# Kernel optimization log

Hardware: AMD Instinct MI355X
Metric: run time of the kernel (lower is better)

## Reference

```python
import jax, jax.numpy as jnp
import numpy as np

N = 50000      # number of nodes
D = 128        # embedding dim
K = 16         # padded neighbors per node
B = 100000     # number of train pairs
LAYERS = 2     # convolution layers


def setup_inputs() -> dict:
    key = jax.random.key(0)
    k_pairs, k_lab, k_nbr, k_emb, k_w1, k_w2 = jax.random.split(key, 6)
    pairs = jax.random.randint(k_pairs, (B, 2), 0, N, dtype=jnp.int64 if jax.config.jax_enable_x64 else jnp.int32)
    labels = jax.random.randint(k_lab, (B,), 0, 2, dtype=jnp.int32)
    neighbors = jax.random.randint(k_nbr, (N, K), 0, N, dtype=jnp.int32)
    embedding = jax.random.normal(k_emb, (N, D), dtype=jnp.float32)
    W1 = jax.random.normal(k_w1, (2 * D, D), dtype=jnp.float32) * (1.0 / np.sqrt(2 * D))
    b1 = jnp.zeros((D,), dtype=jnp.float32)
    W2 = jax.random.normal(k_w2, (D, 2), dtype=jnp.float32) * (1.0 / np.sqrt(D))
    b2 = jnp.zeros((2,), dtype=jnp.float32)
    return {"pairs": pairs, "labels": labels, "neighbors": neighbors,
            "embedding": embedding, "W1": W1, "b1": b1, "W2": W2, "b2": b2}


def _aggregate(embedding, neighbors):
    # Multi-layer mean neighbor aggregation over all N nodes.
    H = embedding
    for _ in range(LAYERS):
        # gather [N, K, D] then mean over neighbors -> [N, D]
        H = jnp.take(H, neighbors, axis=0).mean(axis=1)
    return H


def reference(pairs, labels, neighbors, embedding, W1, b1, W2, b2):
    H = _aggregate(embedding, neighbors)           # [N, D]
    src = jnp.take(H, pairs[:, 0], axis=0)         # [B, D]
    dst = jnp.take(H, pairs[:, 1], axis=0)         # [B, D]
    x = jnp.concatenate([src, dst], axis=-1)       # [B, 2D]
    h = jax.nn.relu(x @ W1 + b1)                   # [B, D]
    logits = h @ W2 + b2                           # [B, 2]
    # Original applies Softmax, then CrossEntropyLoss (which log_softmaxes again).
    probs = jax.nn.softmax(logits, axis=-1)
    logp = jax.nn.log_softmax(probs, axis=-1)
    loss = -jnp.take_along_axis(logp, labels[:, None].astype(jnp.int32), axis=1).mean()
    return loss
```

## Files before the change

### kernel.cpp

```cpp
#include <hip/hip_runtime.h>
#include <hip/hip_bf16.h>

#define NNODES 50000
#define DIM    128
#define KNBR   16
#define NPAIRS 100000
#define MBLK   128

typedef float          f32x4  __attribute__((ext_vector_type(4)));
typedef float          f32x2  __attribute__((ext_vector_type(2)));
typedef __bf16         bf16x8 __attribute__((ext_vector_type(8)));
typedef unsigned short u16x8  __attribute__((ext_vector_type(8)));
typedef unsigned int   u32x2  __attribute__((ext_vector_type(2)));

__device__ __forceinline__ unsigned short f2bf(float f) {
    unsigned int u = __builtin_bit_cast(unsigned int, f);
    u = (u + 0x7fffu + ((u >> 16) & 1u)) >> 16;
    return (unsigned short)u;
}

#if __has_builtin(__builtin_amdgcn_cvt_pk_f32_fp8) && __has_builtin(__builtin_amdgcn_cvt_pk_fp8_f32)
template <bool HI>
__device__ __forceinline__ f32x2 fp8x2_dec(unsigned int w) {
    return __builtin_amdgcn_cvt_pk_f32_fp8((int)w, HI);
}
template <bool HI>
__device__ __forceinline__ unsigned int fp8x2_enc(float a, float b, unsigned int old) {
    return (unsigned int)__builtin_amdgcn_cvt_pk_fp8_f32(a, b, (int)old, HI);
}
#else
__device__ __forceinline__ float e4m3_dec1(unsigned int b) {
    unsigned int s = (b & 0x80u) << 24;
    unsigned int em = b & 0x7fu;
    float mag = (em >= 8u)
        ? __builtin_bit_cast(float, (((em >> 3) + 120u) << 23) | ((em & 7u) << 20))
        : (float)em * 0.001953125f;
    return __builtin_bit_cast(float, __builtin_bit_cast(unsigned int, mag) | s);
}
template <bool HI>
__device__ __forceinline__ f32x2 fp8x2_dec(unsigned int w) {
    unsigned int v = HI ? (w >> 16) : w;
    f32x2 r; r[0] = e4m3_dec1(v & 0xffu); r[1] = e4m3_dec1((v >> 8) & 0xffu);
    return r;
}
__device__ __forceinline__ unsigned int e4m3_enc1(float f) {
    unsigned int s = (__builtin_bit_cast(unsigned int, f) >> 24) & 0x80u;
    float af = fminf(fabsf(f), 448.0f);
    unsigned int u = __builtin_bit_cast(unsigned int, af);
    int e = (int)(u >> 23) - 127;
    if (e < -9) return s;
    if (e < -6) {
        int q = (int)rintf(af * 512.0f);
        return s | (unsigned int)q;
    }
    unsigned int mant = u & 0x7fffffu;
    unsigned int r = (mant + 0x7ffffu + ((mant >> 20) & 1u)) >> 20;
    unsigned int out = (((unsigned int)(e + 7)) << 3) + r;
    if (out > 0x7eu) out = 0x7eu;
    return s | out;
}
template <bool HI>
__device__ __forceinline__ unsigned int fp8x2_enc(float a, float b, unsigned int old) {
    unsigned int p = e4m3_enc1(a) | (e4m3_enc1(b) << 8);
    return HI ? ((old & 0x0000ffffu) | (p << 16)) : ((old & 0xffff0000u) | p);
}
#endif

#define AS1 __attribute__((address_space(1)))
#define AS3 __attribute__((address_space(3)))
__device__ __forceinline__ void gload_lds16(const void* g, void* l) {
    __builtin_amdgcn_global_load_lds((AS1 void*)(g), (AS3 void*)(l), 16, 0, 0);
}

__global__ void w1t_kernel(const float* __restrict__ W1, unsigned short* __restrict__ W1t) {
    int g = blockIdx.x * 256 + threadIdx.x;
    int i = g >> 7;
    int d = g & 127;
    W1t[d * 256 + i] = f2bf(W1[g]);
}

__global__ void e2f8_kernel(const float* __restrict__ E, unsigned int* __restrict__ E8) {
    int g = blockIdx.x * 256 + threadIdx.x;
    const f32x4 v0 = *(const f32x4*)(E + (size_t)g * 8);
    const f32x4 v1 = *(const f32x4*)(E + (size_t)g * 8 + 4);
    unsigned int w0 = 0, w1 = 0;
    w0 = fp8x2_enc<false>(v0[0], v0[1], w0);
    w0 = fp8x2_enc<true >(v0[2], v0[3], w0);
    w1 = fp8x2_enc<false>(v1[0], v1[1], w1);
    w1 = fp8x2_enc<true >(v1[2], v1[3], w1);
    u32x2 o; o[0] = w0; o[1] = w1;
    *(u32x2*)(E8 + (size_t)g * 2) = o;
}

__global__ void agg1_kernel(const unsigned char* __restrict__ E8, const int* __restrict__ nbr,
                            unsigned char* __restrict__ H1f8) {
    int t = threadIdx.x;
    int node = blockIdx.x * 16 + (t >> 4);
    int c = t & 15;
    const int* nl = nbr + node * KNBR;
    float a[8] = {0.f,0.f,0.f,0.f,0.f,0.f,0.f,0.f};
#pragma unroll
    for (int k = 0; k < KNBR; ++k) {
        const u32x2 w = *(const u32x2*)(E8 + (size_t)nl[k] * 128 + c * 8);
        f32x2 f;
        f = fp8x2_dec<false>(w[0]); a[0] += f[0]; a[1] += f[1];
        f = fp8x2_dec<true >(w[0]); a[2] += f[0]; a[3] += f[1];
        f = fp8x2_dec<false>(w[1]); a[4] += f[0]; a[5] += f[1];
        f = fp8x2_dec<true >(w[1]); a[6] += f[0]; a[7] += f[1];
    }
    unsigned int w0 = 0, w1 = 0;
    w0 = fp8x2_enc<false>(a[0] * 0.0625f, a[1] * 0.0625f, w0);
    w0 = fp8x2_enc<true >(a[2] * 0.0625f, a[3] * 0.0625f, w0);
    w1 = fp8x2_enc<false>(a[4] * 0.0625f, a[5] * 0.0625f, w1);
    w1 = fp8x2_enc<true >(a[6] * 0.0625f, a[7] * 0.0625f, w1);
    u32x2 o; o[0] = w0; o[1] = w1;
    *(u32x2*)(H1f8 + (size_t)node * 128 + c * 8) = o;
}

__global__ void agg2_kernel(const unsigned char* __restrict__ H1f8, const int* __restrict__ nbr,
                            unsigned short* __restrict__ H2b) {
    int t = threadIdx.x;
    int node = blockIdx.x * 16 + (t >> 4);
    int c = t & 15;
    const int* nl = nbr + node * KNBR;
    float a[8] = {0.f,0.f,0.f,0.f,0.f,0.f,0.f,0.f};
#pragma unroll
    for (int k = 0; k < KNBR; ++k) {
        const u32x2 w = *(const u32x2*)(H1f8 + (size_t)nl[k] * 128 + c * 8);
        f32x2 f;
        f = fp8x2_dec<false>(w[0]); a[0] += f[0]; a[1] += f[1];
        f = fp8x2_dec<true >(w[0]); a[2] += f[0]; a[3] += f[1];
        f = fp8x2_dec<false>(w[1]); a[4] += f[0]; a[5] += f[1];
        f = fp8x2_dec<true >(w[1]); a[6] += f[0]; a[7] += f[1];
    }
    u16x8 o;
#pragma unroll
    for (int j = 0; j < 8; ++j) o[j] = f2bf(a[j] * 0.0625f);
    *(u16x8*)(H2b + (size_t)node * DIM + c * 8) = o;
}

__global__ __launch_bounds__(256, 2) void pair_mlp_kernel(
    const int* __restrict__ pairs, const int* __restrict__ labels,
    const unsigned short* __restrict__ H2b, const unsigned short* __restrict__ W1t,
    const float* __restrict__ b1, const float* __restrict__ W2,
    const float* __restrict__ b2, float* __restrict__ out) {
    __shared__ unsigned short As[MBLK * 256];
    __shared__ float LP[4][MBLK][2];
    __shared__ float wred[4];

    const int t    = threadIdx.x;
    const int wave = t >> 6;
    const int lane = t & 63;
    const int base = blockIdx.x * MBLK;

    const int lq = (lane & 31) * 16;
    const int lr = lane >> 5;

#pragma unroll
    for (int i = 0; i < 16; ++i) {
        int m0 = wave * 32 + i * 2;
        int m  = m0 + lr;
        int b  = lq ^ ((m & 7) << 4);
        int half = lq >> 8;
        int pm = base + m; if (pm >= NPAIRS) pm = NPAIRS - 1;
        int node = pairs[pm * 2 + half];
        gload_lds16((const char*)H2b + (size_t)node * 256 + (b & 255),
                    (char*)As + m0 * 512);
    }

    const int lg = lane >> 4;
    const int ll = lane & 15;
    const int col0 = wave * 32 + ll;
    const int col1 = col0 + 16;
    bf16x8 breg0[8], breg1[8];
#pragma unroll
    for (int ks = 0; ks < 8; ++ks) {
        const int kb = ks * 64 + lg * 16;
        breg0[ks] = *(const bf16x8*)((const char*)W1t + col0 * 512 + kb);
        breg1[ks] = *(const bf16x8*)((const char*)W1t + col1 * 512 + kb);
    }
    __syncthreads();

    f32x4 acc[8][2];
    {
        f32x4 z = {0.f, 0.f, 0.f, 0.f};
#pragma unroll
        for (int i = 0; i < 8; ++i) { acc[i][0] = z; acc[i][1] = z; }
    }
#pragma unroll
    for (int ks = 0; ks < 8; ++ks) {
        const int kb = ks * 64 + lg * 16;
#pragma unroll
        for (int mf = 0; mf < 8; ++mf) {
            int row = mf * 16 + ll;
            bf16x8 af = *(const bf16x8*)((const char*)As + row * 512 + (kb ^ ((row & 7) << 4)));
            acc[mf][0] = __builtin_amdgcn_mfma_f32_16x16x32_bf16(af, breg0[ks], acc[mf][0], 0, 0, 0);
            acc[mf][1] = __builtin_amdgcn_mfma_f32_16x16x32_bf16(af, breg1[ks], acc[mf][1], 0, 0, 0);
        }
    }

    {
        const float b1v0 = b1[col0], b1v1 = b1[col1];
        const float w2a0 = W2[col0 * 2], w2b0 = W2[col0 * 2 + 1];
        const float w2a1 = W2[col1 * 2], w2b1 = W2[col1 * 2 + 1];
#pragma unroll
        for (int mf = 0; mf < 8; ++mf) {
            float p0[4], p1[4];
#pragma unroll
            for (int r = 0; r < 4; ++r) {
                float h0 = fmaxf(acc[mf][0][r] + b1v0, 0.f);
                float h1 = fmaxf(acc[mf][1][r] + b1v1, 0.f);
                p0[r] = h0 * w2a0 + h1 * w2a1;
                p1[r] = h0 * w2b0 + h1 * w2b1;
            }
#pragma unroll
            for (int s = 1; s < 16; s <<= 1) {
#pragma unroll
                for (int r = 0; r < 4; ++r) {
                    p0[r] += __shfl_xor(p0[r], s, 16);
                    p1[r] += __shfl_xor(p1[r], s, 16);
                }
            }
            if (ll == 0) {
                int rb = mf * 16 + lg * 4;
#pragma unroll
                for (int r = 0; r < 4; ++r) {
                    LP[wave][rb + r][0] = p0[r];
                    LP[wave][rb + r][1] = p1[r];
                }
            }
        }
    }
    __syncthreads();

    float myloss = 0.f;
    if (t < MBLK) {
        int pm = base + t;
        if (pm < NPAIRS) {
            float l0 = b2[0] + LP[0][t][0] + LP[1][t][0] + LP[2][t][0] + LP[3][t][0];
            float l1 = b2[1] + LP[0][t][1] + LP[1][t][1] + LP[2][t][1] + LP[3][t][1];
            float mx = fmaxf(l0, l1);
            float e0 = __expf(l0 - mx), e1 = __expf(l1 - mx);
            float inv = 1.f / (e0 + e1);
            float q0 = e0 * inv, q1 = e1 * inv;
            float lse2 = __logf(__expf(q0) + __expf(q1));
            myloss = lse2 - (labels[pm] ? q1 : q0);
        }
    }
#pragma unroll
    for (int s = 1; s < 64; s <<= 1) myloss += __shfl_xor(myloss, s, 64);
    if (lane == 0) wred[wave] = myloss;
    __syncthreads();
    if (t == 0)
        atomicAdd(out, (wred[0] + wred[1] + wred[2] + wred[3]) * (1.0f / (float)NPAIRS));
}

extern "C" void kernel_launch(void* const* d_in, const int* in_sizes, int n_in,
                              void* d_out, int out_size, void* d_ws, size_t ws_size,
                              hipStream_t stream) {
    const int*   pairs  = (const int*)d_in[0];
    const int*   labels = (const int*)d_in[1];
    const int*   nbr    = (const int*)d_in[2];
    const float* E      = (const float*)d_in[3];
    const float* W1     = (const float*)d_in[4];
    const float* b1     = (const float*)d_in[5];
    const float* W2     = (const float*)d_in[6];
    const float* b2     = (const float*)d_in[7];
    float* out = (float*)d_out;

    char* ws = (char*)d_ws;
    unsigned short* W1t  = (unsigned short*)(ws);
    unsigned char*  E8   = (unsigned char*)(ws + 65536);
    unsigned char*  H1f8 = E8 + (size_t)NNODES * DIM;
    unsigned short* H2b  = (unsigned short*)(H1f8 + (size_t)NNODES * DIM);

    (void)hipMemsetAsync(out, 0, sizeof(float), stream);

    w1t_kernel<<<dim3(128), dim3(256), 0, stream>>>(W1, W1t);
    e2f8_kernel<<<dim3((NNODES * DIM) / (256 * 8)), dim3(256), 0, stream>>>(E, (unsigned int*)E8);
    agg1_kernel<<<dim3(NNODES / 16), dim3(256), 0, stream>>>(E8, nbr, H1f8);
    agg2_kernel<<<dim3(NNODES / 16), dim3(256), 0, stream>>>(H1f8, nbr, H2b);
    pair_mlp_kernel<<<dim3((NPAIRS + MBLK - 1) / MBLK), dim3(256), 0, stream>>>(
        pairs, labels, H2b, W1t, b1, W2, b2, out);
}
```

Measured before the change: 144.6 us.

## Persist pair MLP blocks with double-buffered gathers; stage aggregation rows through LDS

The pair MLP kernel becomes persistent: 512 blocks each loop over 64-pair tiles. The next tile's H2 row gather goes into a second LDS buffer while MFMAs run on the current one, and W1 is loaded into registers once per block instead of once per tile. The aggregation kernels now issue all neighbor row loads as asynchronous global-to-LDS copies before any accumulation, so more loads are in flight per wave. The cost is extra LDS, more barriers per tile and added per-block control logic.

```diff
diff --git a/kernel.cpp b/kernel.cpp
--- a/kernel.cpp
+++ b/kernel.cpp
@@ -5,13 +5,16 @@
 #define DIM    128
 #define KNBR   16
 #define NPAIRS 100000
-#define MBLK   128
+#define MBLK   64
+#define NT     1563
+#define GRID_P 512
 
 typedef float          f32x4  __attribute__((ext_vector_type(4)));
 typedef float          f32x2  __attribute__((ext_vector_type(2)));
 typedef __bf16         bf16x8 __attribute__((ext_vector_type(8)));
 typedef unsigned short u16x8  __attribute__((ext_vector_type(8)));
 typedef unsigned int   u32x2  __attribute__((ext_vector_type(2)));
+typedef unsigned int   u32x4  __attribute__((ext_vector_type(4)));
 
 __device__ __forceinline__ unsigned short f2bf(float f) {
     unsigned int u = __builtin_bit_cast(unsigned int, f);
@@ -49,10 +52,7 @@
     unsigned int u = __builtin_bit_cast(unsigned int, af);
     int e = (int)(u >> 23) - 127;
     if (e < -9) return s;
-    if (e < -6) {
-        int q = (int)rintf(af * 512.0f);
-        return s | (unsigned int)q;
-    }
+    if (e < -6) { int q = (int)rintf(af * 512.0f); return s | (unsigned int)q; }
     unsigned int mant = u & 0x7fffffu;
     unsigned int r = (mant + 0x7ffffu + ((mant >> 20) & 1u)) >> 20;
     unsigned int out = (((unsigned int)(e + 7)) << 3) + r;
@@ -92,51 +92,67 @@
     *(u32x2*)(E8 + (size_t)g * 2) = o;
 }
 
-__global__ void agg1_kernel(const unsigned char* __restrict__ E8, const int* __restrict__ nbr,
-                            unsigned char* __restrict__ H1f8) {
-    int t = threadIdx.x;
-    int node = blockIdx.x * 16 + (t >> 4);
-    int c = t & 15;
-    const int* nl = nbr + node * KNBR;
-    float a[8] = {0.f,0.f,0.f,0.f,0.f,0.f,0.f,0.f};
+__device__ __forceinline__ void agg_core(const unsigned char* __restrict__ T,
+                                         const int* __restrict__ nbr,
+                                         unsigned char* lds_wave,
+                                         int node_base,
+                                         int lane, float* a ) {
+    const int rsub = lane >> 3;
+    const int bcol = (lane & 7) * 16;
+    const int* nb = nbr + node_base * KNBR;
+#pragma unroll
+    for (int i = 0; i < 8; ++i) {
+        int nl = nb[i * 8 + rsub];
+        gload_lds16(T + (size_t)nl * 128 + bcol, lds_wave + i * 1024);
+    }
+    asm volatile("s_waitcnt vmcnt(0)" ::: "memory");
+    __builtin_amdgcn_sched_barrier(0);
+    const int g = lane >> 4;
+    const int c = lane & 15;
+#pragma unroll
+    for (int j = 0; j < 8; ++j) a[j] = 0.f;
 #pragma unroll
     for (int k = 0; k < KNBR; ++k) {
-        const u32x2 w = *(const u32x2*)(E8 + (size_t)nl[k] * 128 + c * 8);
+        const u32x2 v = *(const u32x2*)(lds_wave + (g * 16 + k) * 128 + c * 8);
         f32x2 f;
-        f = fp8x2_dec<false>(w[0]); a[0] += f[0]; a[1] += f[1];
-        f = fp8x2_dec<true >(w[0]); a[2] += f[0]; a[3] += f[1];
-        f = fp8x2_dec<false>(w[1]); a[4] += f[0]; a[5] += f[1];
-        f = fp8x2_dec<true >(w[1]); a[6] += f[0]; a[7] += f[1];
-    }
-    unsigned int w0 = 0, w1 = 0;
-    w0 = fp8x2_enc<false>(a[0] * 0.0625f, a[1] * 0.0625f, w0);
-    w0 = fp8x2_enc<true >(a[2] * 0.0625f, a[3] * 0.0625f, w0);
-    w1 = fp8x2_enc<false>(a[4] * 0.0625f, a[5] * 0.0625f, w1);
-    w1 = fp8x2_enc<true >(a[6] * 0.0625f, a[7] * 0.0625f, w1);
-    u32x2 o; o[0] = w0; o[1] = w1;
-    *(u32x2*)(H1f8 + (size_t)node * 128 + c * 8) = o;
-}
-
-__global__ void agg2_kernel(const unsigned char* __restrict__ H1f8, const int* __restrict__ nbr,
-                            unsigned short* __restrict__ H2b) {
-    int t = threadIdx.x;
-    int node = blockIdx.x * 16 + (t >> 4);
-    int c = t & 15;
-    const int* nl = nbr + node * KNBR;
-    float a[8] = {0.f,0.f,0.f,0.f,0.f,0.f,0.f,0.f};
-#pragma unroll
-    for (int k = 0; k < KNBR; ++k) {
-        const u32x2 w = *(const u32x2*)(H1f8 + (size_t)nl[k] * 128 + c * 8);
-        f32x2 f;
-        f = fp8x2_dec<false>(w[0]); a[0] += f[0]; a[1] += f[1];
-        f = fp8x2_dec<true >(w[0]); a[2] += f[0]; a[3] += f[1];
-        f = fp8x2_dec<false>(w[1]); a[4] += f[0]; a[5] += f[1];
-        f = fp8x2_dec<true >(w[1]); a[6] += f[0]; a[7] += f[1];
-    }
+        f = fp8x2_dec<false>(v[0]); a[0] += f[0]; a[1] += f[1];
+        f = fp8x2_dec<true >(v[0]); a[2] += f[0]; a[3] += f[1];
+        f = fp8x2_dec<false>(v[1]); a[4] += f[0]; a[5] += f[1];
+        f = fp8x2_dec<true >(v[1]); a[6] += f[0]; a[7] += f[1];
+    }
+}
+
+__global__ __launch_bounds__(256) void agg1_kernel(const unsigned char* __restrict__ E8,
+                                                   const int* __restrict__ nbr,
+                                                   unsigned char* __restrict__ H1f8) {
+    __shared__ unsigned char SL[4][8192];
+    const int t = threadIdx.x, wave = t >> 6, lane = t & 63;
+    const int node_base = blockIdx.x * 16 + wave * 4;
+    float a[8];
+    agg_core(E8, nbr, SL[wave], node_base, lane, a);
+    const int g = lane >> 4, c = lane & 15;
+    unsigned int o0 = 0, o1 = 0;
+    o0 = fp8x2_enc<false>(a[0] * 0.0625f, a[1] * 0.0625f, o0);
+    o0 = fp8x2_enc<true >(a[2] * 0.0625f, a[3] * 0.0625f, o0);
+    o1 = fp8x2_enc<false>(a[4] * 0.0625f, a[5] * 0.0625f, o1);
+    o1 = fp8x2_enc<true >(a[6] * 0.0625f, a[7] * 0.0625f, o1);
+    u32x2 o; o[0] = o0; o[1] = o1;
+    *(u32x2*)(H1f8 + (size_t)(node_base + g) * 128 + c * 8) = o;
+}
+
+__global__ __launch_bounds__(256) void agg2_kernel(const unsigned char* __restrict__ H1f8,
+                                                   const int* __restrict__ nbr,
+                                                   unsigned short* __restrict__ H2b) {
+    __shared__ unsigned char SL[4][8192];
+    const int t = threadIdx.x, wave = t >> 6, lane = t & 63;
+    const int node_base = blockIdx.x * 16 + wave * 4;
+    float a[8];
+    agg_core(H1f8, nbr, SL[wave], node_base, lane, a);
+    const int g = lane >> 4, c = lane & 15;
     u16x8 o;
 #pragma unroll
     for (int j = 0; j < 8; ++j) o[j] = f2bf(a[j] * 0.0625f);
-    *(u16x8*)(H2b + (size_t)node * DIM + c * 8) = o;
+    *(u16x8*)(H2b + (size_t)(node_base + g) * DIM + c * 8) = o;
 }
 
 __global__ __launch_bounds__(256, 2) void pair_mlp_kernel(
@@ -144,34 +160,37 @@
     const unsigned short* __restrict__ H2b, const unsigned short* __restrict__ W1t,
     const float* __restrict__ b1, const float* __restrict__ W2,
     const float* __restrict__ b2, float* __restrict__ out) {
-    __shared__ unsigned short As[MBLK * 256];
+    __shared__ unsigned short As[2][MBLK * 256];
     __shared__ float LP[4][MBLK][2];
     __shared__ float wred[4];
 
-    const int t    = threadIdx.x;
-    const int wave = t >> 6;
-    const int lane = t & 63;
-    const int base = blockIdx.x * MBLK;
-
-    const int lq = (lane & 31) * 16;
-    const int lr = lane >> 5;
-
-#pragma unroll
-    for (int i = 0; i < 16; ++i) {
-        int m0 = wave * 32 + i * 2;
-        int m  = m0 + lr;
-        int b  = lq ^ ((m & 7) << 4);
-        int half = lq >> 8;
-        int pm = base + m; if (pm >= NPAIRS) pm = NPAIRS - 1;
-        int node = pairs[pm * 2 + half];
-        gload_lds16((const char*)H2b + (size_t)node * 256 + (b & 255),
-                    (char*)As + m0 * 512);
-    }
-
-    const int lg = lane >> 4;
-    const int ll = lane & 15;
+    const int tid  = threadIdx.x;
+    const int wave = tid >> 6;
+    const int lane = tid & 63;
+    const int bid  = blockIdx.x;
+
+    const int lq   = (lane & 31) * 16;
+    const int lr   = lane >> 5;
+    const int half = lq >> 8;
+    const int lg   = lane >> 4;
+    const int ll   = lane & 15;
     const int col0 = wave * 32 + ll;
     const int col1 = col0 + 16;
+    const int myN  = (NT - bid + GRID_P - 1) / GRID_P;
+
+    const float b1v0 = b1[col0], b1v1 = b1[col1];
+    const float w2a0 = W2[col0 * 2], w2b0 = W2[col0 * 2 + 1];
+    const float w2a1 = W2[col1 * 2], w2b1 = W2[col1 * 2 + 1];
+    const float b20 = b2[0], b21 = b2[1];
+    int lab[4] = {0, 0, 0, 0};
+#pragma unroll
+    for (int j = 0; j < 4; ++j) {
+        int tt = bid + j * GRID_P;
+        if (tt < NT && tid < MBLK) {
+            int pm = tt * MBLK + tid;
+            if (pm < NPAIRS) lab[j] = labels[pm];
+        }
+    }
     bf16x8 breg0[8], breg1[8];
 #pragma unroll
     for (int ks = 0; ks < 8; ++ks) {
@@ -179,32 +198,67 @@
         breg0[ks] = *(const bf16x8*)((const char*)W1t + col0 * 512 + kb);
         breg1[ks] = *(const bf16x8*)((const char*)W1t + col1 * 512 + kb);
     }
-    __syncthreads();
-
-    f32x4 acc[8][2];
-    {
-        f32x4 z = {0.f, 0.f, 0.f, 0.f};
-#pragma unroll
-        for (int i = 0; i < 8; ++i) { acc[i][0] = z; acc[i][1] = z; }
-    }
-#pragma unroll
-    for (int ks = 0; ks < 8; ++ks) {
-        const int kb = ks * 64 + lg * 16;
-#pragma unroll
-        for (int mf = 0; mf < 8; ++mf) {
-            int row = mf * 16 + ll;
-            bf16x8 af = *(const bf16x8*)((const char*)As + row * 512 + (kb ^ ((row & 7) << 4)));
-            acc[mf][0] = __builtin_amdgcn_mfma_f32_16x16x32_bf16(af, breg0[ks], acc[mf][0], 0, 0, 0);
-            acc[mf][1] = __builtin_amdgcn_mfma_f32_16x16x32_bf16(af, breg1[ks], acc[mf][1], 0, 0, 0);
-        }
-    }
-
-    {
-        const float b1v0 = b1[col0], b1v1 = b1[col1];
-        const float w2a0 = W2[col0 * 2], w2b0 = W2[col0 * 2 + 1];
-        const float w2a1 = W2[col1 * 2], w2b1 = W2[col1 * 2 + 1];
-#pragma unroll
-        for (int mf = 0; mf < 8; ++mf) {
+#pragma unroll
+    for (int i = 0; i < 8; ++i) {
+        int m0 = wave * 16 + i * 2;
+        int m  = m0 + lr;
+        int b  = lq ^ ((m & 7) << 4);
+        int pm = bid * MBLK + m; if (pm >= NPAIRS) pm = NPAIRS - 1;
+        int node = pairs[pm * 2 + half];
+        gload_lds16((const char*)H2b + (size_t)node * 256 + (b & 255),
+                    (char*)&As[0][0] + m0 * 512);
+    }
+
+    float lacc = 0.f;
+#pragma unroll
+    for (int j = 0; j < 4; ++j) {
+        const int t = bid + j * GRID_P;
+        if (t >= NT) break;
+        int tn = t + GRID_P; if (tn >= NT) tn = t;
+        const int cur = j & 1;
+
+        asm volatile("s_waitcnt vmcnt(0)" ::: "memory");
+        __builtin_amdgcn_sched_barrier(0);
+        __builtin_amdgcn_s_barrier();
+        __builtin_amdgcn_sched_barrier(0);
+
+        int nd[8];
+#pragma unroll
+        for (int i = 0; i < 8; ++i) {
+            int m  = wave * 16 + i * 2 + lr;
+            int pm = tn * MBLK + m; if (pm >= NPAIRS) pm = NPAIRS - 1;
+            nd[i] = pairs[pm * 2 + half];
+        }
+
+        f32x4 acc[4][2];
+        {
+            f32x4 z = {0.f, 0.f, 0.f, 0.f};
+#pragma unroll
+            for (int i = 0; i < 4; ++i) { acc[i][0] = z; acc[i][1] = z; }
+        }
+#pragma unroll
+        for (int ks = 0; ks < 8; ++ks) {
+            const int kb = ks * 64 + lg * 16;
+#pragma unroll
+            for (int mf = 0; mf < 4; ++mf) {
+                int row = mf * 16 + ll;
+                bf16x8 af = *(const bf16x8*)((const char*)&As[cur][0] + row * 512 + (kb ^ ((row & 7) << 4)));
+                acc[mf][0] = __builtin_amdgcn_mfma_f32_16x16x32_bf16(af, breg0[ks], acc[mf][0], 0, 0, 0);
+                acc[mf][1] = __builtin_amdgcn_mfma_f32_16x16x32_bf16(af, breg1[ks], acc[mf][1], 0, 0, 0);
+            }
+        }
+
+#pragma unroll
+        for (int i = 0; i < 8; ++i) {
+            int m0 = wave * 16 + i * 2;
+            int m  = m0 + lr;
+            int b  = lq ^ ((m & 7) << 4);
+            gload_lds16((const char*)H2b + (size_t)nd[i] * 256 + (b & 255),
+                        (char*)&As[cur ^ 1][0] + m0 * 512);
+        }
+
+#pragma unroll
+        for (int mf = 0; mf < 4; ++mf) {
             float p0[4], p1[4];
 #pragma unroll
             for (int r = 0; r < 4; ++r) {
@@ -230,28 +284,32 @@
                 }
             }
         }
-    }
+        asm volatile("s_waitcnt lgkmcnt(0)" ::: "memory");
+        __builtin_amdgcn_sched_barrier(0);
+        __builtin_amdgcn_s_barrier();
+        __builtin_amdgcn_sched_barrier(0);
+
+        if (tid < MBLK) {
+            int pm = t * MBLK + tid;
+            if (pm < NPAIRS) {
+                float l0 = b20 + LP[0][tid][0] + LP[1][tid][0] + LP[2][tid][0] + LP[3][tid][0];
+                float l1 = b21 + LP[0][tid][1] + LP[1][tid][1] + LP[2][tid][1] + LP[3][tid][1];
+                float mx = fmaxf(l0, l1);
+                float e0 = __expf(l0 - mx), e1 = __expf(l1 - mx);
+                float inv = 1.f / (e0 + e1);
+                float q0 = e0 * inv, q1 = e1 * inv;
+                float lse2 = __logf(__expf(q0) + __expf(q1));
+                lacc += lse2 - (lab[j] ? q1 : q0);
+            }
+        }
+    }
+
     __syncthreads();
-
-    float myloss = 0.f;
-    if (t < MBLK) {
-        int pm = base + t;
-        if (pm < NPAIRS) {
-            float l0 = b2[0] + LP[0][t][0] + LP[1][t][0] + LP[2][t][0] + LP[3][t][0];
-            float l1 = b2[1] + LP[0][t][1] + LP[1][t][1] + LP[2][t][1] + LP[3][t][1];
-            float mx = fmaxf(l0, l1);
-            float e0 = __expf(l0 - mx), e1 = __expf(l1 - mx);
-            float inv = 1.f / (e0 + e1);
-            float q0 = e0 * inv, q1 = e1 * inv;
-            float lse2 = __logf(__expf(q0) + __expf(q1));
-            myloss = lse2 - (labels[pm] ? q1 : q0);
-        }
-    }
-#pragma unroll
-    for (int s = 1; s < 64; s <<= 1) myloss += __shfl_xor(myloss, s, 64);
-    if (lane == 0) wred[wave] = myloss;
+#pragma unroll
+    for (int s = 1; s < 64; s <<= 1) lacc += __shfl_xor(lacc, s, 64);
+    if (lane == 0) wred[wave] = lacc;
     __syncthreads();
-    if (t == 0)
+    if (tid == 0)
         atomicAdd(out, (wred[0] + wred[1] + wred[2] + wred[3]) * (1.0f / (float)NPAIRS));
 }
 
@@ -280,6 +338,6 @@
     e2f8_kernel<<<dim3((NNODES * DIM) / (256 * 8)), dim3(256), 0, stream>>>(E, (unsigned int*)E8);
     agg1_kernel<<<dim3(NNODES / 16), dim3(256), 0, stream>>>(E8, nbr, H1f8);
     agg2_kernel<<<dim3(NNODES / 16), dim3(256), 0, stream>>>(H1f8, nbr, H2b);
-    pair_mlp_kernel<<<dim3((NPAIRS + MBLK - 1) / MBLK), dim3(256), 0, stream>>>(
+    pair_mlp_kernel<<<dim3(GRID_P), dim3(256), 0, stream>>>(
         pairs, labels, H2b, W1t, b1, W2, b2, out);
 }
```

Result: faster. 140.3 us (-3.0%).
